# Optimization experiments

Hardware: AMD Instinct MI355X
Metric: run time of the kernel (lower is better)

## Reference

```python
import jax, jax.numpy as jnp
import numpy as np

EPS = 1e-12  # torch F.normalize eps

def _l2norm(t):
    # normalize along last axis, clamp norm like torch.nn.functional.normalize
    n = jnp.sqrt(jnp.sum(t * t, axis=-1, keepdims=True))
    return t / jnp.maximum(n, EPS)

def setup_inputs() -> dict:
    key = jax.random.key(0)
    k1, k2, k3 = jax.random.split(key, 3)
    B, N, C, h = 4, 16384, 512, 8
    x = jax.random.normal(k1, (B, N, C), dtype=jnp.float32)
    qkv_w = jax.random.normal(k2, (C, 3 * C), dtype=jnp.float32) * 0.02
    proj_w = jax.random.normal(k3, (C, C), dtype=jnp.float32) * 0.02
    proj_b = jnp.zeros((C,), dtype=jnp.float32)
    temperature = jnp.ones((h, 1, 1), dtype=jnp.float32)  # temperature_init=1.0
    return {"x": x, "H": 128, "W": 128, "qkv_w": qkv_w,
            "proj_w": proj_w, "proj_b": proj_b, "temperature": temperature}

def reference(x, H, W, qkv_w, proj_w, proj_b, temperature):
    B, N, C = x.shape
    h = temperature.shape[0]
    d = C // h
    qkv = (x @ qkv_w).reshape(B, N, 3, h, d)          # [B,N,3,h,d]
    qkv = jnp.transpose(qkv, (2, 0, 3, 1, 4))         # [3,B,h,N,d]
    q, k, v = qkv[0], qkv[1], qkv[2]
    # channel attention: transpose to [B,h,d,N], normalize over tokens
    q = _l2norm(jnp.swapaxes(q, -2, -1))              # [B,h,d,N]
    k = _l2norm(jnp.swapaxes(k, -2, -1))              # [B,h,d,N]
    v = jnp.swapaxes(v, -2, -1)                       # [B,h,d,N]
    attn = jnp.einsum('bhdn,bhen->bhde', q, k) * temperature  # [B,h,d,d]
    attn = jax.nn.softmax(attn, axis=-1)
    out = jnp.einsum('bhde,bhen->bhdn', attn, v)      # [B,h,d,N]
    out = jnp.transpose(out, (0, 3, 1, 2)).reshape(B, N, C)
    return out @ proj_w + proj_b
```

## Files before the change

kernel.cpp:

```cpp
#include <hip/hip_runtime.h>
#include <stdint.h>
#include <stddef.h>


typedef unsigned short u16;
typedef __attribute__((ext_vector_type(8))) unsigned short u16x8;
typedef __attribute__((ext_vector_type(8))) __bf16 bf16x8;
typedef __attribute__((ext_vector_type(4))) float f32x4;

#define B_DIM 4
#define N_TOK 16384
#define C_DIM 512
#define CQ3   1536
#define NROWS 65536

__constant__ int PTI[10] = {0, 0, 0, 0, 1, 1, 1, 2, 2, 3};
__constant__ int PTJ[10] = {0, 1, 2, 3, 1, 2, 3, 2, 3, 3};
__constant__ int OTI[6] = {0, 0, 0, 1, 1, 2};
__constant__ int OTJ[6] = {1, 2, 3, 2, 3, 3};

__device__ __forceinline__ u16 f2bf(float f) {
  union { float f; uint32_t u; } v; v.f = f;
  uint32_t r = v.u + 0x7FFFu + ((v.u >> 16) & 1u);
  return (u16)(r >> 16);
}
__device__ __forceinline__ float bf2f(u16 u) {
  union { uint32_t u; float f; } v; v.u = ((uint32_t)u) << 16;
  return v.f;
}
__device__ __forceinline__ bf16x8 as_bf16x8(u16x8 u) {
  union { u16x8 u; bf16x8 b; } v; v.u = u; return v.b;
}
__device__ __forceinline__ bf16x8 ldfrag(const u16* p) {
  return as_bf16x8(*(const u16x8*)p);
}
__device__ __forceinline__ void gl_lds16(const void* g, void* l) {
  __builtin_amdgcn_global_load_lds(
      (const __attribute__((address_space(1))) uint32_t*)g,
      (__attribute__((address_space(3))) uint32_t*)l, 16, 0, 0);
}
#define VMDRAIN asm volatile("s_waitcnt vmcnt(0)" ::: "memory")

__global__ __launch_bounds__(256) void k_prep(const float* __restrict__ qkv_w,
                                              const float* __restrict__ proj_w,
                                              u16* __restrict__ wl,
                                              u16* __restrict__ pwl,
                                              u16* __restrict__ vA) {
  int g = blockIdx.x * 256 + threadIdx.x;
  if (g < 98304) {
    int c8 = g / CQ3, j = g - c8 * CQ3;
    u16x8 o;
#pragma unroll
    for (int i = 0; i < 8; ++i) o[i] = f2bf(qkv_w[(size_t)(c8 * 8 + i) * CQ3 + j]);
    *(u16x8*)(wl + (size_t)g * 8) = o;
  } else if (g < 131072) {
    int gg = g - 98304;
    int d8 = gg >> 9, j = gg & 511;
    u16x8 o;
#pragma unroll
    for (int i = 0; i < 8; ++i) o[i] = f2bf(proj_w[(size_t)(d8 * 8 + i) * 512 + j]);
    *(u16x8*)(pwl + (size_t)gg * 8) = o;
  } else {
    int gg = g - 131072;
    int c = gg >> 6, q = gg & 63;
    const float* s = qkv_w + (size_t)c * CQ3 + 1024 + q * 8;
    float4 v0 = *(const float4*)s, v1 = *(const float4*)(s + 4);
    u16x8 o;
    o[0] = f2bf(v0.x); o[1] = f2bf(v0.y); o[2] = f2bf(v0.z); o[3] = f2bf(v0.w);
    o[4] = f2bf(v1.x); o[5] = f2bf(v1.y); o[6] = f2bf(v1.z); o[7] = f2bf(v1.w);
    *(u16x8*)(vA + (size_t)gg * 8) = o;
  }
}

__global__ __launch_bounds__(256) void k_xc(const float* __restrict__ x,
                                            u16* __restrict__ xb,
                                            u16* __restrict__ xbT) {
  __shared__ __align__(16) u16 T[16384];
  const int bi = blockIdx.x;
  const int b = bi >> 9, tt = (bi >> 2) & 127, ct = bi & 3;
  const int n0 = tt * 128, c0 = ct * 128;
  const int tid = threadIdx.x;
  const int cb8 = (tid & 15) * 8;
  const int tch = tid >> 4;
  const float* src = x + (size_t)(b * N_TOK + n0 + tch * 8) * C_DIM + c0 + cb8;
  float v[8][8];
#pragma unroll
  for (int j = 0; j < 8; ++j) {
    float4 a0 = *(const float4*)(src + (size_t)j * C_DIM);
    float4 a1 = *(const float4*)(src + (size_t)j * C_DIM + 4);
    v[j][0] = a0.x; v[j][1] = a0.y; v[j][2] = a0.z; v[j][3] = a0.w;
    v[j][4] = a1.x; v[j][5] = a1.y; v[j][6] = a1.z; v[j][7] = a1.w;
  }
  u16* xbd = xb + (size_t)(b * N_TOK + n0 + tch * 8) * C_DIM + c0 + cb8;
#pragma unroll
  for (int j = 0; j < 8; ++j) {
    u16x8 o;
#pragma unroll
    for (int i = 0; i < 8; ++i) o[i] = f2bf(v[j][i]);
    *(u16x8*)(xbd + (size_t)j * C_DIM) = o;
  }
#pragma unroll
  for (int i = 0; i < 8; ++i) {
    int c_loc = cb8 + i;
    int pc = tch ^ (tid & 15);
    u16x8 o;
#pragma unroll
    for (int j = 0; j < 8; ++j) o[j] = f2bf(v[j][i]);
    *(u16x8*)&T[c_loc * 128 + pc * 8] = o;
  }
  __syncthreads();
#pragma unroll
  for (int t = 0; t < 8; ++t) {
    int c_loc = t * 16 + (tid >> 4);
    int lch = tid & 15;
    int pc = lch ^ ((c_loc >> 3) & 15);
    u16x8 o = *(const u16x8*)&T[c_loc * 128 + pc * 8];
    *(u16x8*)&xbT[(size_t)(b * C_DIM + c0 + c_loc) * N_TOK + n0 + lch * 8] = o;
  }
}

__global__ __launch_bounds__(256) void k_g(const u16* __restrict__ xbT, u16* __restrict__ Gp) {
  __shared__ __align__(16) u16 As[2][8192];
  __shared__ __align__(16) u16 Bs[2][8192];
  const int tid = threadIdx.x, lane = tid & 63, wid = tid >> 6;
  const int orig = blockIdx.x;
  const int wg = (orig & 7) * 80 + (orig >> 3);
  const int kc = wg / 40, rem = wg % 40;
  const int b = rem / 10, p = rem % 10;
  const int ti = PTI[p], tj = PTJ[p];
  const u16* abase = xbT + ((size_t)b * 512 + ti * 128) * N_TOK + kc * 1024;
  const u16* bbase = xbT + ((size_t)b * 512 + tj * 128) * N_TOK + kc * 1024;
  const int wr = wid >> 1, wc = wid & 1;

  auto stage = [&](int kb, int buf) {
#pragma unroll
    for (int s4 = 0; s4 < 4; ++s4) {
      int slot = s4 * 256 + tid;
      int idx = slot >> 3, kblk = slot & 7;
      int kcol = kb * 64 + ((kblk ^ (idx & 7)) * 8);
      gl_lds16(abase + (size_t)idx * N_TOK + kcol, &As[buf][slot * 8]);
      gl_lds16(bbase + (size_t)idx * N_TOK + kcol, &Bs[buf][slot * 8]);
    }
  };

  f32x4 acc[4][4];
#pragma unroll
  for (int i = 0; i < 4; ++i)
#pragma unroll
    for (int j = 0; j < 4; ++j) acc[i][j] = (f32x4){0.f, 0.f, 0.f, 0.f};

  stage(0, 0);
  VMDRAIN;
  __syncthreads();
  for (int kb = 0; kb < 16; ++kb) {
    const int cur = kb & 1;
    if (kb < 15) stage(kb + 1, cur ^ 1);
#pragma unroll
    for (int kk = 0; kk < 2; ++kk) {
      const int krow = kk * 4 + (lane >> 4);
      const int pk = krow ^ (lane & 7);
      bf16x8 af[4], bfr[4];
#pragma unroll
      for (int t = 0; t < 4; ++t)
        af[t] = *(const bf16x8*)&As[cur][((wr * 64 + t * 16 + (lane & 15)) * 8 + pk) * 8];
#pragma unroll
      for (int t = 0; t < 4; ++t)
        bfr[t] = *(const bf16x8*)&Bs[cur][((wc * 64 + t * 16 + (lane & 15)) * 8 + pk) * 8];
#pragma unroll
      for (int mt = 0; mt < 4; ++mt)
#pragma unroll
        for (int nt = 0; nt < 4; ++nt)
          acc[mt][nt] = __builtin_amdgcn_mfma_f32_16x16x32_bf16(af[mt], bfr[nt], acc[mt][nt], 0, 0, 0);
    }
    if (kb < 15) VMDRAIN;
    __syncthreads();
  }
  u16* wsl = &As[0][0] + wid * 4096;
#pragma unroll
  for (int mt = 0; mt < 4; ++mt)
#pragma unroll
    for (int nt = 0; nt < 4; ++nt)
#pragma unroll
      for (int r = 0; r < 4; ++r) {
        int row = mt * 16 + (lane >> 4) * 4 + r;
        int col = nt * 16 + (lane & 15);
        int slot = (col >> 3) ^ (row & 7);
        wsl[row * 64 + slot * 8 + (col & 7)] = f2bf(acc[mt][nt][r]);
      }
  u16* gdst = Gp + (size_t)(kc * 4 + b) * 262144;
#pragma unroll
  for (int it = 0; it < 8; ++it) {
    int rr = it * 8 + (lane >> 3);
    int slot = (lane & 7) ^ (rr & 7);
    *(u16x8*)&gdst[(size_t)(ti * 128 + wr * 64 + rr) * 512 + tj * 128 + wc * 64 + (lane & 7) * 8] =
        *(const u16x8*)&wsl[rr * 64 + slot * 8];
  }
}

__global__ __launch_bounds__(256) void k_red(const u16* __restrict__ Gp, u16* __restrict__ G) {
  const int bi = blockIdx.x;
  const int b = bi / 80, rem = bi % 80;
  const int p = rem >> 3, sl = rem & 7;
  const int ti = PTI[p], tj = PTJ[p];
  const int tid = threadIdx.x;
  const int row = sl * 16 + (tid >> 4);
  const int c0 = (tid & 15) * 8;
  const size_t off = (size_t)(ti * 128 + row) * 512 + tj * 128 + c0;
  float s[8];
#pragma unroll
  for (int i = 0; i < 8; ++i) s[i] = 0.f;
  const u16* src = Gp + (size_t)b * 262144 + off;
#pragma unroll 4
  for (int kc = 0; kc < 16; ++kc) {
    u16x8 v = *(const u16x8*)(src + (size_t)kc * 1048576);
#pragma unroll
    for (int i = 0; i < 8; ++i) s[i] += bf2f(v[i]);
  }
  u16x8 o;
#pragma unroll
  for (int i = 0; i < 8; ++i) o[i] = f2bf(s[i]);
  *(u16x8*)(G + (size_t)b * 262144 + off) = o;
}

__global__ __launch_bounds__(256) void k_mir(u16* __restrict__ G) {
  __shared__ u16 T[128][130];
  const int bi = blockIdx.x;
  const int b = bi / 6, q = bi - b * 6;
  const int ti = OTI[q], tj = OTJ[q];
  const int tid = threadIdx.x;
  const int r = tid >> 1, h = tid & 1;
  u16* gb = G + (size_t)b * 262144;
#pragma unroll
  for (int c8 = 0; c8 < 8; ++c8) {
    u16x8 v = *(const u16x8*)(gb + (size_t)(ti * 128 + r) * 512 + tj * 128 + h * 64 + c8 * 8);
#pragma unroll
    for (int i = 0; i < 8; ++i) T[r][h * 64 + c8 * 8 + i] = v[i];
  }
  __syncthreads();
#pragma unroll
  for (int c8 = 0; c8 < 8; ++c8) {
    int d0 = h * 64 + c8 * 8;
    u16x8 o;
#pragma unroll
    for (int i = 0; i < 8; ++i) o[i] = T[d0 + i][r];
    *(u16x8*)(gb + (size_t)(tj * 128 + r) * 512 + ti * 128 + d0) = o;
  }
}

__global__ __launch_bounds__(256) void k_gq(const u16* __restrict__ G,
                                            const u16* __restrict__ wl,
                                            u16* __restrict__ Gqk) {
  const int bi = blockIdx.x;
  const int b = bi >> 5, mt = (bi >> 3) & 3, nt2 = bi & 7;
  const int m0 = mt * 128, n0 = nt2 * 128;
  const int lane = threadIdx.x & 63, w = threadIdx.x >> 6;
  f32x4 acc[8][2];
#pragma unroll
  for (int i = 0; i < 8; ++i) { acc[i][0] = (f32x4){0,0,0,0}; acc[i][1] = (f32x4){0,0,0,0}; }
  for (int ks = 0; ks < 16; ++ks) {
    bf16x8 bfr[2];
#pragma unroll
    for (int nf = 0; nf < 2; ++nf)
      bfr[nf] = ldfrag(wl + ((size_t)(ks * 4 + (lane >> 4)) * CQ3 + n0 + w * 32 + nf * 16 + (lane & 15)) * 8);
#pragma unroll
    for (int mf = 0; mf < 8; ++mf) {
      bf16x8 af = ldfrag(G + (size_t)b * 262144 + (size_t)(m0 + mf * 16 + (lane & 15)) * 512 + ks * 32 + (lane >> 4) * 8);
#pragma unroll
      for (int nf = 0; nf < 2; ++nf)
        acc[mf][nf] = __builtin_amdgcn_mfma_f32_16x16x32_bf16(af, bfr[nf], acc[mf][nf], 0, 0, 0);
    }
  }
#pragma unroll
  for (int mf = 0; mf < 8; ++mf)
#pragma unroll
    for (int nf = 0; nf < 2; ++nf)
#pragma unroll
      for (int r = 0; r < 4; ++r) {
        int d = m0 + mf * 16 + (lane >> 4) * 4 + r;
        int j = n0 + w * 32 + nf * 16 + (lane & 15);
        Gqk[(size_t)b * 524288 + ((size_t)(d >> 3) * 1024 + j) * 8 + (d & 7)] = f2bf(acc[mf][nf][r]);
      }
}

__global__ __launch_bounds__(256) void k_s2(const u16* __restrict__ Gqk,
                                            const u16* __restrict__ wl,
                                            const u16* __restrict__ pwl,
                                            const float* __restrict__ temp,
                                            u16* __restrict__ Ml) {
  __shared__ float Ssh[4][4096];
  __shared__ u16 At[64 * 72];
  __shared__ float ssqsh[128];
  __shared__ float rqk[128];
  const int tid = threadIdx.x, lane = tid & 63, w = tid >> 6;
  const int bh = blockIdx.x, b = bh >> 3, hh = bh & 7;
  if (tid < 128) ssqsh[tid] = 0.f;

  f32x4 acc[4][4];
#pragma unroll
  for (int i = 0; i < 4; ++i)
#pragma unroll
    for (int j = 0; j < 4; ++j) acc[i][j] = (f32x4){0.f, 0.f, 0.f, 0.f};
  for (int ks = 0; ks < 4; ++ks) {
    const int crow = w * 16 + ks * 4 + (lane >> 4);
    bf16x8 aq[4], bk[4];
#pragma unroll
    for (int mf = 0; mf < 4; ++mf)
      aq[mf] = ldfrag(wl + ((size_t)crow * CQ3 + hh * 64 + mf * 16 + (lane & 15)) * 8);
#pragma unroll
    for (int nf = 0; nf < 4; ++nf)
      bk[nf] = ldfrag(Gqk + (size_t)b * 524288 + ((size_t)crow * 1024 + 512 + hh * 64 + nf * 16 + (lane & 15)) * 8);
#pragma unroll
    for (int mf = 0; mf < 4; ++mf)
#pragma unroll
      for (int nf = 0; nf < 4; ++nf)
        acc[mf][nf] = __builtin_amdgcn_mfma_f32_16x16x32_bf16(aq[mf], bk[nf], acc[mf][nf], 0, 0, 0);
  }
#pragma unroll
  for (int mf = 0; mf < 4; ++mf)
#pragma unroll
    for (int nf = 0; nf < 4; ++nf)
#pragma unroll
      for (int r = 0; r < 4; ++r)
        Ssh[w][(mf * 16 + (lane >> 4) * 4 + r) * 64 + nf * 16 + (lane & 15)] = acc[mf][nf][r];
  __syncthreads();
  for (int idx = tid; idx < 4096; idx += 256)
    Ssh[0][idx] = Ssh[0][idx] + Ssh[1][idx] + Ssh[2][idx] + Ssh[3][idx];

  {
    const int d = tid & 63, part = tid >> 6;
    float sq = 0.f, sk = 0.f;
    for (int co = 0; co < 16; ++co) {
      int c8 = part * 16 + co;
      u16x8 wq = *(const u16x8*)(wl + ((size_t)c8 * CQ3 + hh * 64 + d) * 8);
      u16x8 gq = *(const u16x8*)(Gqk + (size_t)b * 524288 + ((size_t)c8 * 1024 + hh * 64 + d) * 8);
      u16x8 wk = *(const u16x8*)(wl + ((size_t)c8 * CQ3 + 512 + hh * 64 + d) * 8);
      u16x8 gk = *(const u16x8*)(Gqk + (size_t)b * 524288 + ((size_t)c8 * 1024 + 512 + hh * 64 + d) * 8);
#pragma unroll
      for (int i = 0; i < 8; ++i) {
        sq += bf2f(wq[i]) * bf2f(gq[i]);
        sk += bf2f(wk[i]) * bf2f(gk[i]);
      }
    }
    atomicAdd(&ssqsh[d], sq);
    atomicAdd(&ssqsh[64 + d], sk);
  }
  __syncthreads();
  if (tid < 128) rqk[tid] = 1.f / fmaxf(sqrtf(fmaxf(ssqsh[tid], 0.f)), 1e-12f);
  __syncthreads();

  {
    const float tp = temp[hh];
    const int d = tid >> 2, q4 = tid & 3;
    float vals[16];
    float mx = -3.0e38f;
    const float rqd = rqk[d];
#pragma unroll
    for (int i = 0; i < 16; ++i) {
      float v = Ssh[0][d * 64 + q4 * 16 + i] * rqd * rqk[64 + q4 * 16 + i] * tp;
      vals[i] = v; mx = fmaxf(mx, v);
    }
    mx = fmaxf(mx, __shfl_xor(mx, 1));
    mx = fmaxf(mx, __shfl_xor(mx, 2));
    float sum = 0.f;
#pragma unroll
    for (int i = 0; i < 16; ++i) { vals[i] = __expf(vals[i] - mx); sum += vals[i]; }
    sum += __shfl_xor(sum, 1);
    sum += __shfl_xor(sum, 2);
    const float inv = 1.f / sum;
#pragma unroll
    for (int i = 0; i < 16; ++i) At[(q4 * 16 + i) * 72 + d] = f2bf(vals[i] * inv);
  }
  __syncthreads();

  f32x4 acc2[4][8];
#pragma unroll
  for (int i = 0; i < 4; ++i)
#pragma unroll
    for (int j = 0; j < 8; ++j) acc2[i][j] = (f32x4){0.f, 0.f, 0.f, 0.f};
#pragma unroll
  for (int s = 0; s < 2; ++s) {
    bf16x8 af[4], bfr[8];
#pragma unroll
    for (int mf = 0; mf < 4; ++mf)
      af[mf] = *(const bf16x8*)&At[(mf * 16 + (lane & 15)) * 72 + s * 32 + (lane >> 4) * 8];
#pragma unroll
    for (int nf = 0; nf < 8; ++nf)
      bfr[nf] = ldfrag(pwl + ((size_t)(hh * 8 + s * 4 + (lane >> 4)) * 512 + w * 128 + nf * 16 + (lane & 15)) * 8);
#pragma unroll
    for (int mf = 0; mf < 4; ++mf)
#pragma unroll
      for (int nf = 0; nf < 8; ++nf)
        acc2[mf][nf] = __builtin_amdgcn_mfma_f32_16x16x32_bf16(af[mf], bfr[nf], acc2[mf][nf], 0, 0, 0);
  }
#pragma unroll
  for (int mf = 0; mf < 4; ++mf)
#pragma unroll
    for (int nf = 0; nf < 8; ++nf)
#pragma unroll
      for (int r = 0; r < 4; ++r) {
        int e = mf * 16 + (lane >> 4) * 4 + r;
        int j = w * 128 + nf * 16 + (lane & 15);
        int cc = hh * 64 + e;
        Ml[(size_t)b * 262144 + ((size_t)(cc >> 3) * 512 + j) * 8 + (cc & 7)] = f2bf(acc2[mf][nf][r]);
      }
}

__global__ __launch_bounds__(256) void k_p(const u16* __restrict__ vA,
                                           const u16* __restrict__ Ml,
                                           u16* __restrict__ Pl) {
  const int bi = blockIdx.x;
  const int b = bi >> 4, ct = (bi >> 2) & 3, jt = bi & 3;
  const int m0 = ct * 128, j0 = jt * 128;
  const int lane = threadIdx.x & 63, w = threadIdx.x >> 6;
  f32x4 acc[8][2];
#pragma unroll
  for (int i = 0; i < 8; ++i) { acc[i][0] = (f32x4){0,0,0,0}; acc[i][1] = (f32x4){0,0,0,0}; }
  for (int ks = 0; ks < 16; ++ks) {
    bf16x8 bfr[2];
#pragma unroll
    for (int nf = 0; nf < 2; ++nf)
      bfr[nf] = ldfrag(Ml + (size_t)b * 262144 + ((size_t)(ks * 4 + (lane >> 4)) * 512 + j0 + w * 32 + nf * 16 + (lane & 15)) * 8);
#pragma unroll
    for (int mf = 0; mf < 8; ++mf) {
      bf16x8 af = ldfrag(vA + (size_t)(m0 + mf * 16 + (lane & 15)) * 512 + ks * 32 + (lane >> 4) * 8);
#pragma unroll
      for (int nf = 0; nf < 2; ++nf)
        acc[mf][nf] = __builtin_amdgcn_mfma_f32_16x16x32_bf16(af, bfr[nf], acc[mf][nf], 0, 0, 0);
    }
  }
#pragma unroll
  for (int mf = 0; mf < 8; ++mf)
#pragma unroll
    for (int nf = 0; nf < 2; ++nf)
#pragma unroll
      for (int r = 0; r < 4; ++r) {
        int c = m0 + mf * 16 + (lane >> 4) * 4 + r;
        int j = j0 + w * 32 + nf * 16 + (lane & 15);
        Pl[(size_t)b * 262144 + ((size_t)(c >> 3) * 512 + j) * 8 + (c & 7)] = f2bf(acc[mf][nf][r]);
      }
}

__global__ __launch_bounds__(256, 4) void k_out(const u16* __restrict__ xb,
                                                const u16* __restrict__ Pl,
                                                const float* __restrict__ pb,
                                                float* __restrict__ out) {
  __shared__ __align__(16) u16 As[8192];
  __shared__ __align__(16) u16 Bs[8192];
  const int tid = threadIdx.x;
  const int orig = blockIdx.x;
  const int wg = (orig & 7) * 256 + (orig >> 3);
  const int cb = wg & 3, rb = wg >> 2;
  const int row0 = rb * 128, col0 = cb * 128;
  const int b = rb >> 7;
  const int lane = tid & 63, wid = tid >> 6;
  const int wr = wid >> 1, wc = wid & 1;
  float bias[4];
#pragma unroll
  for (int nt = 0; nt < 4; ++nt) bias[nt] = pb[col0 + wc * 64 + nt * 16 + (lane & 15)];

  f32x4 acc[4][4];
#pragma unroll
  for (int i = 0; i < 4; ++i)
#pragma unroll
    for (int j = 0; j < 4; ++j) acc[i][j] = (f32x4){0.f, 0.f, 0.f, 0.f};

  const u16* pbase = Pl + (size_t)b * 262144;
  for (int kb = 0; kb < 8; ++kb) {
#pragma unroll
    for (int s4 = 0; s4 < 4; ++s4) {
      int slot = s4 * 256 + tid;
      int idx = slot >> 3, kblk = slot & 7;
      gl_lds16(xb + (size_t)(row0 + idx) * C_DIM + kb * 64 + ((kblk ^ (idx & 7)) * 8), &As[slot * 8]);
      int kblkB = slot >> 7, j = slot & 127;
      gl_lds16(pbase + ((size_t)(kb * 8 + kblkB) * 512 + col0 + j) * 8, &Bs[slot * 8]);
    }
    __syncthreads();
#pragma unroll
    for (int kk = 0; kk < 2; ++kk) {
      const int krow = kk * 4 + (lane >> 4);
      const int pk = krow ^ (lane & 7);
      bf16x8 af[4], bfr[4];
#pragma unroll
      for (int t = 0; t < 4; ++t)
        af[t] = *(const bf16x8*)&As[((wr * 64 + t * 16 + (lane & 15)) * 8 + pk) * 8];
#pragma unroll
      for (int t = 0; t < 4; ++t)
        bfr[t] = *(const bf16x8*)&Bs[(krow * 128 + wc * 64 + t * 16 + (lane & 15)) * 8];
#pragma unroll
      for (int mt = 0; mt < 4; ++mt)
#pragma unroll
        for (int nt = 0; nt < 4; ++nt)
          acc[mt][nt] = __builtin_amdgcn_mfma_f32_16x16x32_bf16(af[mt], bfr[nt], acc[mt][nt], 0, 0, 0);
    }
    __syncthreads();
  }
  float* slice = (wid < 2) ? (float*)&As[wid * 4096] : (float*)&Bs[(wid - 2) * 4096];
#pragma unroll
  for (int half = 0; half < 2; ++half) {
#pragma unroll
    for (int m2 = 0; m2 < 2; ++m2)
#pragma unroll
      for (int nt = 0; nt < 4; ++nt)
#pragma unroll
        for (int r = 0; r < 4; ++r) {
          int row = m2 * 16 + (lane >> 4) * 4 + r;
          int col = nt * 16 + (lane & 15);
          int slot = (col >> 2) ^ (row & 15);
          slice[row * 64 + slot * 4 + (col & 3)] = acc[half * 2 + m2][nt][r] + bias[nt];
        }
#pragma unroll
    for (int it = 0; it < 8; ++it) {
      int rr = it * 4 + (lane >> 4);
      int s = (lane & 15) ^ (rr & 15);
      *(float4*)&out[(size_t)(row0 + wr * 64 + half * 32 + rr) * C_DIM + col0 + wc * 64 + (lane & 15) * 4] =
          *(const float4*)&slice[rr * 64 + s * 4];
    }
  }
}

extern "C" void kernel_launch(void* const* d_in, const int* in_sizes, int n_in,
                              void* d_out, int out_size, void* d_ws, size_t ws_size,
                              hipStream_t stream) {
  const float* x      = (const float*)d_in[0];
  const float* qkv_w  = (const float*)d_in[3];
  const float* proj_w = (const float*)d_in[4];
  const float* proj_b = (const float*)d_in[5];
  const float* temp   = (const float*)d_in[6];
  float* out = (float*)d_out;

  char* ws = (char*)d_ws;
  u16* xb  = (u16*)(ws);
  u16* xbT = (u16*)(ws + 67108864);
  u16* wl  = (u16*)(ws + 134217728);
  u16* pwl = (u16*)(ws + 135790592);
  u16* vA  = (u16*)(ws + 136314880);
  u16* Gp  = (u16*)(ws + 136839168);
  u16* G   = (u16*)(ws + 170393600);
  u16* Gqk = (u16*)(ws + 172490752);
  u16* Ml  = (u16*)(ws + 176685056);
  u16* Pl  = (u16*)(ws + 178782208);

  k_xc<<<2048, 256, 0, stream>>>(x, xb, xbT);
  k_prep<<<640, 256, 0, stream>>>(qkv_w, proj_w, wl, pwl, vA);
  k_g<<<640, 256, 0, stream>>>(xbT, Gp);
  k_red<<<320, 256, 0, stream>>>(Gp, G);
  k_mir<<<24, 256, 0, stream>>>(G);
  k_gq<<<128, 256, 0, stream>>>(G, wl, Gqk);
  k_s2<<<32, 256, 0, stream>>>(Gqk, wl, pwl, temp, Ml);
  k_p<<<64, 256, 0, stream>>>(vA, Ml, Pl);
  k_out<<<2048, 256, 0, stream>>>(xb, Pl, proj_b, out);
}
```

Measured before the change: 245.6 us.

## Fuse Gram mirroring into reduction and prefetch xb into L2 during k_p

Removes the separate k_mir launch by having k_red write each off-diagonal Gram tile's transpose directly with scalar scattered stores. It also launches k_p with extra blocks that only stream-read the bf16 x buffer, with the sums discarded, so the data is warm in cache for k_out. The scattered transposed stores are uncoalesced. The prefetch blocks add memory traffic and may compete with the small k_p GEMM or be ineffective if the buffer exceeds cache capacity.

```diff
diff --git a/kernel.cpp b/kernel.cpp
--- a/kernel.cpp
+++ b/kernel.cpp
@@ -16,8 +16,6 @@
 
 __constant__ int PTI[10] = {0, 0, 0, 0, 1, 1, 1, 2, 2, 3};
 __constant__ int PTJ[10] = {0, 1, 2, 3, 1, 2, 3, 2, 3, 3};
-__constant__ int OTI[6] = {0, 0, 0, 1, 1, 2};
-__constant__ int OTJ[6] = {1, 2, 3, 2, 3, 3};
 
 __device__ __forceinline__ u16 f2bf(float f) {
   union { float f; uint32_t u; } v; v.f = f;
@@ -219,31 +217,12 @@
   u16x8 o;
 #pragma unroll
   for (int i = 0; i < 8; ++i) o[i] = f2bf(s[i]);
-  *(u16x8*)(G + (size_t)b * 262144 + off) = o;
-}
-
-__global__ __launch_bounds__(256) void k_mir(u16* __restrict__ G) {
-  __shared__ u16 T[128][130];
-  const int bi = blockIdx.x;
-  const int b = bi / 6, q = bi - b * 6;
-  const int ti = OTI[q], tj = OTJ[q];
-  const int tid = threadIdx.x;
-  const int r = tid >> 1, h = tid & 1;
   u16* gb = G + (size_t)b * 262144;
-#pragma unroll
-  for (int c8 = 0; c8 < 8; ++c8) {
-    u16x8 v = *(const u16x8*)(gb + (size_t)(ti * 128 + r) * 512 + tj * 128 + h * 64 + c8 * 8);
-#pragma unroll
-    for (int i = 0; i < 8; ++i) T[r][h * 64 + c8 * 8 + i] = v[i];
-  }
-  __syncthreads();
-#pragma unroll
-  for (int c8 = 0; c8 < 8; ++c8) {
-    int d0 = h * 64 + c8 * 8;
-    u16x8 o;
-#pragma unroll
-    for (int i = 0; i < 8; ++i) o[i] = T[d0 + i][r];
-    *(u16x8*)(gb + (size_t)(tj * 128 + r) * 512 + ti * 128 + d0) = o;
+  *(u16x8*)(gb + off) = o;
+  if (ti != tj) {
+#pragma unroll
+    for (int i = 0; i < 8; ++i)
+      gb[(size_t)(tj * 128 + c0 + i) * 512 + ti * 128 + row] = o[i];
   }
 }
 
@@ -407,8 +386,20 @@
 
 __global__ __launch_bounds__(256) void k_p(const u16* __restrict__ vA,
                                            const u16* __restrict__ Ml,
-                                           u16* __restrict__ Pl) {
+                                           u16* __restrict__ Pl,
+                                           const u16* __restrict__ xb) {
   const int bi = blockIdx.x;
+  if (bi >= 64) {
+    const float4* p = (const float4*)xb;
+    float sx = 0.f, sy = 0.f, sz = 0.f, sw = 0.f;
+    for (size_t i = (size_t)(bi - 64) * 256 + threadIdx.x; i < 4194304;
+         i += (size_t)1984 * 256) {
+      float4 v = p[i];
+      sx += v.x; sy += v.y; sz += v.z; sw += v.w;
+    }
+    asm volatile("" :: "v"(sx), "v"(sy), "v"(sz), "v"(sw));
+    return;
+  }
   const int b = bi >> 4, ct = (bi >> 2) & 3, jt = bi & 3;
   const int m0 = ct * 128, j0 = jt * 128;
   const int lane = threadIdx.x & 63, w = threadIdx.x >> 6;
@@ -544,9 +535,8 @@
   k_prep<<<640, 256, 0, stream>>>(qkv_w, proj_w, wl, pwl, vA);
   k_g<<<640, 256, 0, stream>>>(xbT, Gp);
   k_red<<<320, 256, 0, stream>>>(Gp, G);
-  k_mir<<<24, 256, 0, stream>>>(G);
   k_gq<<<128, 256, 0, stream>>>(G, wl, Gqk);
   k_s2<<<32, 256, 0, stream>>>(Gqk, wl, pwl, temp, Ml);
-  k_p<<<64, 256, 0, stream>>>(vA, Ml, Pl);
+  k_p<<<2048, 256, 0, stream>>>(vA, Ml, Pl, xb);
   k_out<<<2048, 256, 0, stream>>>(xb, Pl, proj_b, out);
 }
```

Result: faster. 223.3 us (-9.1%).
